# Performance work log

Measured on AMD Instinct MI355X. Metric: run time of the kernel, lower is better.

## Reference

```python
import jax, jax.numpy as jnp
import numpy as np
from jax import lax

WIN = 7            # win_size -> (7,7,7) window in 3d mode
NPIX = WIN ** 3    # 343
K1, K2 = 0.01, 0.03
COV_NORM = NPIX / (NPIX - 1)
DN = ('NCDHW', 'OIDHW', 'NCDHW')


def _box3d(x):
    """Separable uniform (box) mean filter, VALID padding. Same math as
    conv3d with a ones(wt,ws,ws)/NPIX kernel, but O(win) per voxel per axis."""
    kd = jnp.ones((1, 1, WIN, 1, 1), x.dtype)
    kh = jnp.ones((1, 1, 1, WIN, 1), x.dtype)
    kw = jnp.ones((1, 1, 1, 1, WIN), x.dtype)
    x = lax.conv_general_dilated(x, kd, (1, 1, 1), 'VALID', dimension_numbers=DN)
    x = lax.conv_general_dilated(x, kh, (1, 1, 1), 'VALID', dimension_numbers=DN)
    x = lax.conv_general_dilated(x, kw, (1, 1, 1), 'VALID', dimension_numbers=DN)
    return x / NPIX


def setup_inputs() -> dict:
    key = jax.random.key(0)
    k1, k2, k3 = jax.random.split(key, 3)
    shape = (4, 1, 32, 320, 320)  # [B, C=1, T, H, W]
    pred = jax.random.normal(k1, shape, dtype=jnp.float32)
    targ = jax.random.normal(k2, shape, dtype=jnp.float32)
    data_range = jax.random.uniform(k3, (4,), dtype=jnp.float32)
    return {'pred': pred, 'targ': targ, 'data_range': data_range}


def reference(pred, targ, data_range):
    dr = data_range[:, None, None, None, None].astype(pred.dtype)
    C1 = (K1 * dr) ** 2
    C2 = (K2 * dr) ** 2
    ux = _box3d(pred)
    uy = _box3d(targ)
    uxx = _box3d(pred * pred)
    uyy = _box3d(targ * targ)
    uxy = _box3d(pred * targ)
    vx = COV_NORM * (uxx - ux * ux)
    vy = COV_NORM * (uyy - uy * uy)
    vxy = COV_NORM * (uxy - ux * uy)
    A1 = 2 * ux * uy + C1
    A2 = 2 * vxy + C2
    B1 = ux ** 2 + uy ** 2 + C1
    B2 = vx + vy + C2
    S = (A1 * A2) / (B1 * B2)
    return (1 - S).mean()
```

## Files before the change

kernel.cpp:

```cpp
#include <hip/hip_runtime.h>


#define NPIX 343

constexpr int B = 4, T = 32, H = 320, W = 320;
constexpr int TO = T - 6, HO = H - 6, WO = W - 6;
constexpr long long NOUT = (long long)B * TO * HO * WO;

constexpr int TH = 16, TW = 26;
constexpr int IH = 22, IW = 32;
constexpr int NTH = 20, NTW = 13;
constexpr int NS = 32;

__global__ __launch_bounds__(256) void ssim3d_fused(
    const float* __restrict__ pred,
    const float* __restrict__ targ,
    const float* __restrict__ drange,
    double* __restrict__ acc)
{
    __shared__ float sp[2][IH][IW];
    __shared__ float sq[2][IH][IW];
    __shared__ float wsum[4];

    const int bx = blockIdx.x;
    const int b  = bx / (NTH * NTW);
    int rem      = bx % (NTH * NTW);
    const int h0 = (rem / NTW) * TH;
    const int w0 = (rem % NTW) * TW;

    const int tid = threadIdx.x;
    const int oh  = tid >> 4;
    const int k   = tid & 15;

    const float* pb = pred + (long long)b * T * H * W;
    const float* qb = targ + (long long)b * T * H * W;

    const int  i1  = tid + 256;
    const bool f1  = (i1 >= 352);
    const int  rm1 = i1 - (f1 ? 352 : 0);
    const int  r1  = rm1 >> 4, c1 = rm1 & 15;
    const bool act2 = (tid < 192);
    const int  rm2 = tid + 160;
    const int  r2  = rm2 >> 4, c2 = rm2 & 15;

    const int gr0 = min(h0 + oh, H - 1), gc0 = min(w0 + 2 * k,  W - 2);
    const int gr1 = min(h0 + r1, H - 1), gc1 = min(w0 + 2 * c1, W - 2);
    const int gr2 = min(h0 + r2, H - 1), gc2 = min(w0 + 2 * c2, W - 2);
    const float* gp0 = pb + (long long)gr0 * W + gc0;
    const float* gp1 = (f1 ? qb : pb) + (long long)gr1 * W + gc1;
    const float* gp2 = qb + (long long)gr2 * W + gc2;
    const int o0 = oh * IW + 2 * k;
    const int o1 = r1 * IW + 2 * c1;
    const int o2 = r2 * IW + 2 * c2;

    float2 d0, d1, d2;
    auto prefetchw = [&](int s) {
        const long long so = (long long)s * H * W;
        d0 = *reinterpret_cast<const float2*>(gp0 + so);
        d1 = *reinterpret_cast<const float2*>(gp1 + so);
        if (act2) d2 = *reinterpret_cast<const float2*>(gp2 + so);
    };
    auto commitw = [&](int buf) {
        *reinterpret_cast<float2*>(&sp[buf][0][0] + o0) = d0;
        *reinterpret_cast<float2*>((f1 ? &sq[buf][0][0] : &sp[buf][0][0]) + o1) = d1;
        if (act2) *reinterpret_cast<float2*>(&sq[buf][0][0] + o2) = d2;
    };

    const bool vh = (h0 + oh < HO);
    const bool emitk = (k <= 12);
    const bool vE = vh && emitk && (w0 + 2 * k     < WO);
    const bool vO = vh && emitk && (w0 + 2 * k + 1 < WO);

    const float dr  = drange[b];
    const float C1v = (0.01f * dr) * (0.01f * dr);
    const float C2v = (0.03f * dr) * (0.03f * dr);
    const float inv  = 1.0f / (float)NPIX;
    const float covn = (float)NPIX / (float)(NPIX - 1);

    float rE[4][7], rO[4][7], tE[4], tO[4];
#pragma unroll
    for (int f = 0; f < 4; ++f) {
        tE[f] = tO[f] = 0.f;
#pragma unroll
        for (int j = 0; j < 7; ++j) { rE[f][j] = rO[f][j] = 0.f; }
    }
    float loss = 0.f;

    auto ssim1 = [&](const float* tt) {
        float ux  = tt[0] * inv, uy = tt[1] * inv;
        float u2  = tt[2] * inv, uxy = tt[3] * inv;
        float B2 = covn * (u2 - ux * ux - uy * uy) + C2v;
        float A2 = 2.f * covn * (uxy - ux * uy) + C2v;
        float A1 = 2.f * ux * uy + C1v;
        float B1 = ux * ux + uy * uy + C1v;
        return 1.f - __fdividef(A1 * A2, B1 * B2);
    };

    prefetchw(0);
    commitw(0);
    prefetchw(1);
    __syncthreads();

    for (int a = 0; a < NS; a += 7) {
#pragma unroll
        for (int jj = 0; jj < 7; ++jj) {
            const int s = a + jj;
            if (s < NS) {
                const int bs = s & 1, bn = bs ^ 1;

                if (s + 1 < NS) commitw(bn);

                float cA[4] = {0.f, 0.f, 0.f, 0.f};
                float cB[4] = {0.f, 0.f, 0.f, 0.f};
#pragma unroll
                for (int dy = 0; dy < 7; ++dy) {
                    float2 p = *reinterpret_cast<const float2*>(&sp[bs][oh + dy][2 * k]);
                    float2 q = *reinterpret_cast<const float2*>(&sq[bs][oh + dy][2 * k]);
                    cA[0] += p.x;  cB[0] += p.y;
                    cA[1] += q.x;  cB[1] += q.y;
                    cA[2] = fmaf(p.x, p.x, cA[2]);  cA[2] = fmaf(q.x, q.x, cA[2]);
                    cB[2] = fmaf(p.y, p.y, cB[2]);  cB[2] = fmaf(q.y, q.y, cB[2]);
                    cA[3] = fmaf(p.x, q.x, cA[3]);
                    cB[3] = fmaf(p.y, q.y, cB[3]);
                }

                if (s + 2 < NS) prefetchw(s + 2);

                __syncthreads();

                float sEv[4], sOv[4];
#pragma unroll
                for (int f = 0; f < 4; ++f) {
                    float ps = cA[f] + cB[f];
                    float s4 = ps + __shfl_down(ps, 1, 16);
                    float s8 = s4 + __shfl_down(s4, 2, 16);
                    float eH = __shfl_down(cB[f], 3, 16);
                    sEv[f] = s8 - eH;
                    sOv[f] = s8 - cA[f];
                }

#pragma unroll
                for (int f = 0; f < 4; ++f) {
                    tE[f] += sEv[f] - rE[f][jj];  rE[f][jj] = sEv[f];
                    tO[f] += sOv[f] - rO[f][jj];  rO[f][jj] = sOv[f];
                }

                if (s >= 6) {
                    if (vE) loss += ssim1(tE);
                    if (vO) loss += ssim1(tO);
                }
            }
        }
    }

    for (int off = 32; off > 0; off >>= 1)
        loss += __shfl_down(loss, off, 64);
    const int lane = tid & 63;
    const int wid  = tid >> 6;
    if (lane == 0) wsum[wid] = loss;
    __syncthreads();
    if (tid == 0) {
        float s = wsum[0] + wsum[1] + wsum[2] + wsum[3];
        atomicAdd(acc, (double)s);
    }
}

__global__ void ssim3d_finalize(const double* __restrict__ acc,
                                float* __restrict__ out)
{
    out[0] = (float)(acc[0] / (double)NOUT);
}

extern "C" void kernel_launch(void* const* d_in, const int* in_sizes, int n_in,
                              void* d_out, int out_size, void* d_ws, size_t ws_size,
                              hipStream_t stream)
{
    const float* pred   = (const float*)d_in[0];
    const float* targ   = (const float*)d_in[1];
    const float* drange = (const float*)d_in[2];
    float* out  = (float*)d_out;
    double* acc = (double*)d_ws;

    hipMemsetAsync(acc, 0, sizeof(double), stream);

    const int nblocks = B * NTH * NTW;
    ssim3d_fused<<<nblocks, 256, 0, stream>>>(pred, targ, drange, acc);
    ssim3d_finalize<<<1, 1, 0, stream>>>(acc, out);
}
```

Before: 87.85 us.

## Interleave pred/targ into float4 LDS tiles and use DPP row shifts for horizontal sums

```diff
diff --git a/kernel.cpp b/kernel.cpp
--- a/kernel.cpp
+++ b/kernel.cpp
@@ -8,9 +8,15 @@
 constexpr long long NOUT = (long long)B * TO * HO * WO;
 
 constexpr int TH = 16, TW = 26;
-constexpr int IH = 22, IW = 32;
+constexpr int IH = 22, IWP = 16;
 constexpr int NTH = 20, NTW = 13;
 constexpr int NS = 32;
+
+template<int N>
+__device__ __forceinline__ float row_shr(float x) {
+    return __int_as_float(__builtin_amdgcn_update_dpp(
+        0, __float_as_int(x), 0x110 | N, 0xF, 0xF, true));
+}
 
 __global__ __launch_bounds__(256) void ssim3d_fused(
     const float* __restrict__ pred,
@@ -18,8 +24,7 @@
     const float* __restrict__ drange,
     double* __restrict__ acc)
 {
-    __shared__ float sp[2][IH][IW];
-    __shared__ float sq[2][IH][IW];
+    __shared__ float4 spq[2][IH][IWP];
     __shared__ float wsum[4];
 
     const int bx = blockIdx.x;
@@ -35,41 +40,36 @@
     const float* pb = pred + (long long)b * T * H * W;
     const float* qb = targ + (long long)b * T * H * W;
 
-    const int  i1  = tid + 256;
-    const bool f1  = (i1 >= 352);
-    const int  rm1 = i1 - (f1 ? 352 : 0);
-    const int  r1  = rm1 >> 4, c1 = rm1 & 15;
-    const bool act2 = (tid < 192);
-    const int  rm2 = tid + 160;
-    const int  r2  = rm2 >> 4, c2 = rm2 & 15;
+    const int r0 = tid >> 4, c0 = tid & 15;
+    const int gr0 = min(h0 + r0, H - 1), gc0 = min(w0 + 2 * c0, W - 2);
+    const float* g0p = pb + (long long)gr0 * W + gc0;
+    const float* g0q = qb + (long long)gr0 * W + gc0;
 
-    const int gr0 = min(h0 + oh, H - 1), gc0 = min(w0 + 2 * k,  W - 2);
+    const bool act1 = (tid < 96);
+    const int r1 = 16 + (tid >> 4), c1 = tid & 15;
     const int gr1 = min(h0 + r1, H - 1), gc1 = min(w0 + 2 * c1, W - 2);
-    const int gr2 = min(h0 + r2, H - 1), gc2 = min(w0 + 2 * c2, W - 2);
-    const float* gp0 = pb + (long long)gr0 * W + gc0;
-    const float* gp1 = (f1 ? qb : pb) + (long long)gr1 * W + gc1;
-    const float* gp2 = qb + (long long)gr2 * W + gc2;
-    const int o0 = oh * IW + 2 * k;
-    const int o1 = r1 * IW + 2 * c1;
-    const int o2 = r2 * IW + 2 * c2;
+    const float* g1p = pb + (long long)gr1 * W + gc1;
+    const float* g1q = qb + (long long)gr1 * W + gc1;
 
-    float2 d0, d1, d2;
+    float2 d0p, d0q, d1p, d1q;
     auto prefetchw = [&](int s) {
         const long long so = (long long)s * H * W;
-        d0 = *reinterpret_cast<const float2*>(gp0 + so);
-        d1 = *reinterpret_cast<const float2*>(gp1 + so);
-        if (act2) d2 = *reinterpret_cast<const float2*>(gp2 + so);
+        d0p = *reinterpret_cast<const float2*>(g0p + so);
+        d0q = *reinterpret_cast<const float2*>(g0q + so);
+        if (act1) {
+            d1p = *reinterpret_cast<const float2*>(g1p + so);
+            d1q = *reinterpret_cast<const float2*>(g1q + so);
+        }
     };
     auto commitw = [&](int buf) {
-        *reinterpret_cast<float2*>(&sp[buf][0][0] + o0) = d0;
-        *reinterpret_cast<float2*>((f1 ? &sq[buf][0][0] : &sp[buf][0][0]) + o1) = d1;
-        if (act2) *reinterpret_cast<float2*>(&sq[buf][0][0] + o2) = d2;
+        spq[buf][r0][c0] = make_float4(d0p.x, d0p.y, d0q.x, d0q.y);
+        if (act1) spq[buf][r1][c1] = make_float4(d1p.x, d1p.y, d1q.x, d1q.y);
     };
 
     const bool vh = (h0 + oh < HO);
-    const bool emitk = (k <= 12);
-    const bool vE = vh && emitk && (w0 + 2 * k     < WO);
-    const bool vO = vh && emitk && (w0 + 2 * k + 1 < WO);
+    const bool k3 = (k >= 3);
+    const bool vE = k3 && vh && (w0 + 2 * k - 6 < WO);
+    const bool vO = k3 && vh && (w0 + 2 * k - 5 < WO);
 
     const float dr  = drange[b];
     const float C1v = (0.01f * dr) * (0.01f * dr);
@@ -109,22 +109,20 @@
                 const int bs = s & 1, bn = bs ^ 1;
 
                 if (s + 1 < NS) commitw(bn);
+                if (s + 2 < NS) prefetchw(s + 2);
 
                 float cA[4] = {0.f, 0.f, 0.f, 0.f};
                 float cB[4] = {0.f, 0.f, 0.f, 0.f};
 #pragma unroll
                 for (int dy = 0; dy < 7; ++dy) {
-                    float2 p = *reinterpret_cast<const float2*>(&sp[bs][oh + dy][2 * k]);
-                    float2 q = *reinterpret_cast<const float2*>(&sq[bs][oh + dy][2 * k]);
-                    cA[0] += p.x;  cB[0] += p.y;
-                    cA[1] += q.x;  cB[1] += q.y;
-                    cA[2] = fmaf(p.x, p.x, cA[2]);  cA[2] = fmaf(q.x, q.x, cA[2]);
-                    cB[2] = fmaf(p.y, p.y, cB[2]);  cB[2] = fmaf(q.y, q.y, cB[2]);
-                    cA[3] = fmaf(p.x, q.x, cA[3]);
-                    cB[3] = fmaf(p.y, q.y, cB[3]);
+                    float4 v = spq[bs][oh + dy][k];
+                    cA[0] += v.x;  cB[0] += v.y;
+                    cA[1] += v.z;  cB[1] += v.w;
+                    cA[2] = fmaf(v.x, v.x, cA[2]);  cA[2] = fmaf(v.z, v.z, cA[2]);
+                    cB[2] = fmaf(v.y, v.y, cB[2]);  cB[2] = fmaf(v.w, v.w, cB[2]);
+                    cA[3] = fmaf(v.x, v.z, cA[3]);
+                    cB[3] = fmaf(v.y, v.w, cB[3]);
                 }
-
-                if (s + 2 < NS) prefetchw(s + 2);
 
                 __syncthreads();
 
@@ -132,11 +130,11 @@
 #pragma unroll
                 for (int f = 0; f < 4; ++f) {
                     float ps = cA[f] + cB[f];
-                    float s4 = ps + __shfl_down(ps, 1, 16);
-                    float s8 = s4 + __shfl_down(s4, 2, 16);
-                    float eH = __shfl_down(cB[f], 3, 16);
-                    sEv[f] = s8 - eH;
-                    sOv[f] = s8 - cA[f];
+                    float t1 = ps + row_shr<1>(ps);
+                    float s8 = t1 + row_shr<2>(t1);
+                    float eL = row_shr<3>(cA[f]);
+                    sEv[f] = s8 - cB[f];
+                    sOv[f] = s8 - eL;
                 }
 
 #pragma unroll
```

Measured after the change: 74.57 us. 15.1% less time.
